# Kernel optimization log

Measured on AMD Instinct MI355X. Metric: run time of the kernel, lower is better.

## Reference

```python
import jax, jax.numpy as jnp
import numpy as np


def setup_inputs() -> dict:
    key = jax.random.key(0)
    B, L, H, D = 4, 4096, 8, 64
    sample_k = int(np.ceil(np.log(L)))  # factor=1 -> U_part = ceil(ln L_K) = 9
    k1, k2, k3, k4 = jax.random.split(key, 4)
    return {
        "queries": jax.random.normal(k1, (B, L, H, D), jnp.float32),
        "keys": jax.random.normal(k2, (B, L, H, D), jnp.float32),
        "values": jax.random.normal(k3, (B, L, H, D), jnp.float32),
        "index_sample": jax.random.randint(k4, (L, sample_k), 0, L),
    }


def _prob_attention(Q, K, V, index_sample):
    # Q, K, V: [B, H, L, D]
    B, H, L_K, D = K.shape
    L_Q = Q.shape[2]
    u = min(int(np.ceil(np.log(L_Q))), L_Q)  # n_top (static)

    # --- _prob_QK: sampled scores, sparsity measure M, top-u queries ---
    # gather sampled keys per query position: [B, H, L_Q, sample_k, D]
    K_sample = K[:, :, index_sample, :]
    QK_sample = jnp.einsum('bhld,bhlsd->bhls', Q, K_sample)  # [B,H,L_Q,S]
    M = QK_sample.max(axis=-1) - QK_sample.sum(axis=-1) / L_K  # [B,H,L_Q]
    _, M_top = jax.lax.top_k(M, u)  # [B,H,u] indices of top queries

    Q_reduce = jnp.take_along_axis(Q, M_top[..., None], axis=2)  # [B,H,u,D]
    scale = 1.0 / jnp.sqrt(jnp.asarray(D, Q.dtype))
    scores = jnp.einsum('bhud,bhkd->bhuk', Q_reduce, K) * scale  # [B,H,u,L_K]

    # --- initial context (mask_flag=False): mean of V over keys ---
    context = jnp.broadcast_to(V.mean(axis=2, keepdims=True), (B, H, L_Q, D))

    # --- update context at the top-u query positions ---
    attn = jax.nn.softmax(scores, axis=-1)  # [B,H,u,L_K]
    ctx_top = jnp.einsum('bhuk,bhkd->bhud', attn, V)  # [B,H,u,D]
    b_idx = jnp.arange(B)[:, None, None]
    h_idx = jnp.arange(H)[None, :, None]
    context = context.at[b_idx, h_idx, M_top].set(ctx_top)
    return context, attn


def reference(queries, keys, values, index_sample):
    # inputs: [B, L, H, D] -> internal [B, H, L, D]
    Q = queries.transpose(0, 2, 1, 3)
    K = keys.transpose(0, 2, 1, 3)
    V = values.transpose(0, 2, 1, 3)
    context, attn = _prob_attention(Q, K, V, index_sample)
    return context.transpose(0, 2, 1, 3), attn
```

## Files before the change

### kernel.cpp

```cpp
#include <hip/hip_runtime.h>
#include <math.h>

#define B_ 4
#define L_ 4096
#define H_ 8
#define D_ 64
#define S_ 9
#define U_ 9
#define VC_ 64
#define NC_ 32
#define CC_ 16
#define TKC_ 8

#define MBLK_ 2048
#define FILLBLK_ 8192

__device__ __forceinline__ float dot4(const float4& a, const float4& b) {
    return a.x * b.x + a.y * b.y + a.z * b.z + a.w * b.w;
}

__global__ void kernel_M_vmean(const float* __restrict__ Q, const float* __restrict__ K,
                               const int* __restrict__ idx, float* __restrict__ M,
                               const float* __restrict__ V, float* __restrict__ vpart) {
    if (blockIdx.x >= MBLK_) {
        int blk = blockIdx.x - MBLK_;
        int c = blk & (VC_ - 1), b = blk >> 6;
        int col = threadIdx.x & 127;
        int lp  = threadIdx.x >> 7;
        const int CHUNK = L_ / VC_;
        const float4* base = (const float4*)(V + (size_t)b * L_ * H_ * D_);
        float4 acc = make_float4(0.f, 0.f, 0.f, 0.f);
        for (int l = c * CHUNK + lp; l < (c + 1) * CHUNK; l += 2) {
            float4 v = base[(size_t)l * 128 + col];
            acc.x += v.x; acc.y += v.y; acc.z += v.z; acc.w += v.w;
        }
        __shared__ float4 red[256];
        red[threadIdx.x] = acc;
        __syncthreads();
        if (lp == 0) {
            float4 o = red[threadIdx.x + 128];
            acc.x += o.x; acc.y += o.y; acc.z += o.z; acc.w += o.w;
            ((float4*)vpart)[(size_t)blk * 128 + col] = acc;
        }
        return;
    }
    int n = blockIdx.x;
    int x = n & 7, m = n >> 3;
    int chunk = m & 63;
    int bh = (m >> 6) * 8 + x;
    int h = bh & (H_ - 1), b = bh >> 3;
    int t = threadIdx.x;
    int j = t & 3;
    int l = chunk * 64 + (t >> 2);

    int ki[S_];
#pragma unroll
    for (int s = 0; s < S_; ++s) ki[s] = idx[l * S_ + s];

    const float4* qb = (const float4*)(Q + (size_t)((b * L_ + l) * H_ + h) * D_);
    float4 q[4];
#pragma unroll
    for (int c = 0; c < 4; ++c) q[c] = qb[j + 4 * c];

    float dot[S_];
#pragma unroll
    for (int r = 0; r < 3; ++r) {
        const float4* kb0 = (const float4*)(K + (size_t)((b * L_ + ki[3*r+0]) * H_ + h) * D_);
        const float4* kb1 = (const float4*)(K + (size_t)((b * L_ + ki[3*r+1]) * H_ + h) * D_);
        const float4* kb2 = (const float4*)(K + (size_t)((b * L_ + ki[3*r+2]) * H_ + h) * D_);
        float4 kv0[4], kv1[4], kv2[4];
#pragma unroll
        for (int c = 0; c < 4; ++c) {
            kv0[c] = kb0[j + 4 * c];
            kv1[c] = kb1[j + 4 * c];
            kv2[c] = kb2[j + 4 * c];
        }
        float a0 = 0.f, a1 = 0.f, a2 = 0.f;
#pragma unroll
        for (int c = 0; c < 4; ++c) {
            a0 += dot4(q[c], kv0[c]);
            a1 += dot4(q[c], kv1[c]);
            a2 += dot4(q[c], kv2[c]);
        }
        dot[3*r+0] = a0; dot[3*r+1] = a1; dot[3*r+2] = a2;
    }
#pragma unroll
    for (int s = 0; s < S_; ++s) {
        dot[s] += __shfl_xor(dot[s], 1);
        dot[s] += __shfl_xor(dot[s], 2);
    }
    if (j == 0) {
        float mx = -INFINITY, sm = 0.f;
#pragma unroll
        for (int s = 0; s < S_; ++s) { mx = fmaxf(mx, dot[s]); sm += dot[s]; }
        M[((size_t)bh << 12) + l] = mx - sm * (1.0f / (float)L_);
    }
}

#define CSWAP(a, b)                                                          \
    if (v[b] > v[a] || (v[b] == v[a] && id[b] < id[a])) {                    \
        float tv = v[a]; v[a] = v[b]; v[b] = tv;                             \
        int ti = id[a]; id[a] = id[b]; id[b] = ti;                           \
    }

__global__ void kernel_topk1(const float* __restrict__ M,
                             float* __restrict__ cand_v, int* __restrict__ cand_i) {
    int bh = blockIdx.x >> 3;
    int chunk = blockIdx.x & (TKC_ - 1);
    int lane = threadIdx.x;
    const float* Ms = M + ((size_t)bh << 12);

    float v[8]; int id[8];
#pragma unroll
    for (int c = 0; c < 8; ++c) {
        int gi = chunk * 512 + lane + 64 * c;
        v[c] = Ms[gi]; id[c] = gi;
    }
    CSWAP(0,1) CSWAP(2,3) CSWAP(4,5) CSWAP(6,7)
    CSWAP(0,2) CSWAP(1,3) CSWAP(4,6) CSWAP(5,7)
    CSWAP(1,2) CSWAP(5,6)
    CSWAP(0,4) CSWAP(1,5) CSWAP(2,6) CSWAP(3,7)
    CSWAP(2,4) CSWAP(3,5)
    CSWAP(1,2) CSWAP(3,4) CSWAP(5,6)

    float* cv = cand_v + (size_t)blockIdx.x * U_;
    int*   ci = cand_i + (size_t)blockIdx.x * U_;
#pragma unroll
    for (int r = 0; r < U_; ++r) {
        float bv = v[0]; int bi = id[0];
#pragma unroll
        for (int off = 1; off < 64; off <<= 1) {
            float ov = __shfl_xor(bv, off);
            int   oi = __shfl_xor(bi, off);
            if (ov > bv || (ov == bv && oi < bi)) { bv = ov; bi = oi; }
        }
        if (lane == 0) { cv[r] = bv; ci[r] = bi; }
        if (id[0] == bi) {
#pragma unroll
            for (int c = 0; c < 7; ++c) { v[c] = v[c+1]; id[c] = id[c+1]; }
            v[7] = -INFINITY; id[7] = 0x7fffffff;
        }
    }
}

__global__ void kernel_small(const float* __restrict__ cand_v, const int* __restrict__ cand_i,
                             int* __restrict__ Mtop, const float* __restrict__ vpart,
                             float* __restrict__ vmean) {
    if (blockIdx.x >= 32) {
        int bh = blockIdx.x - 32;
        int h = bh & (H_ - 1), b = bh >> 3;
        int d = threadIdx.x;
        float s = 0.0f;
        for (int c = 0; c < VC_; ++c)
            s += vpart[(size_t)(b * VC_ + c) * (H_ * D_) + h * D_ + d];
        vmean[bh * D_ + d] = s * (1.0f / (float)L_);
        return;
    }
    int bh = blockIdx.x;
    int lane = threadIdx.x;
    const float* cv = cand_v + (size_t)bh * (TKC_ * U_);
    const int*   ci = cand_i + (size_t)bh * (TKC_ * U_);

    float v[2]; int id[2];
    v[0] = cv[lane]; id[0] = ci[lane];
    if (lane < TKC_ * U_ - 64) { v[1] = cv[64 + lane]; id[1] = ci[64 + lane]; }
    else { v[1] = -INFINITY; id[1] = 0x7fffffff; }
    CSWAP(0,1)

#pragma unroll
    for (int r = 0; r < U_; ++r) {
        float bv = v[0]; int bi = id[0];
#pragma unroll
        for (int off = 1; off < 64; off <<= 1) {
            float ov = __shfl_xor(bv, off);
            int   oi = __shfl_xor(bi, off);
            if (ov > bv || (ov == bv && oi < bi)) { bv = ov; bi = oi; }
        }
        if (lane == 0) Mtop[bh * U_ + r] = bi;
        if (id[0] == bi) { v[0] = v[1]; id[0] = id[1]; v[1] = -INFINITY; id[1] = 0x7fffffff; }
    }
}

__global__ void kernel_fill_scores(float* __restrict__ out, const float* __restrict__ vmean,
                                   const float* __restrict__ Q, const float* __restrict__ K,
                                   const int* __restrict__ Mtop, float* __restrict__ raw) {
    if (blockIdx.x < FILLBLK_) {
        int i = blockIdx.x * 256 + threadIdx.x;
        int d4 = i & 15;
        int h  = (i >> 4) & (H_ - 1);
        int b  = i >> (4 + 3 + 12);
        ((float4*)out)[i] = ((const float4*)vmean)[(b * H_ + h) * 16 + d4];
        return;
    }
    int n = blockIdx.x - FILLBLK_;
    int x = n & 7, m = n >> 3;
    int chunk = m & (NC_ - 1);
    int bh = (m >> 5) * 8 + x;
    int h = bh & (H_ - 1), b = bh >> 3;
    int k0 = chunk * (L_ / NC_);

    __shared__ float qs[U_][D_];
    int t = threadIdx.x;
    if (t < 144) {
        int u = t / 16, c = t & 15;
        int l = Mtop[bh * U_ + u];
        ((float4*)qs[u])[c] =
            ((const float4*)(Q + (size_t)((b * L_ + l) * H_ + h) * D_))[c];
    }
    __syncthreads();

    int j = t & 3, g = t >> 2;
#pragma unroll
    for (int kk = 0; kk < 2; ++kk) {
        int k = k0 + g + 64 * kk;
        const float4* kb = (const float4*)(K + (size_t)((b * L_ + k) * H_ + h) * D_);
        float4 kv[4];
#pragma unroll
        for (int c = 0; c < 4; ++c) kv[c] = kb[j + 4 * c];
#pragma unroll
        for (int u = 0; u < U_; ++u) {
            float acc = 0.0f;
#pragma unroll
            for (int c = 0; c < 4; ++c)
                acc += dot4(((const float4*)qs[u])[j + 4 * c], kv[c]);
            acc += __shfl_xor(acc, 1);
            acc += __shfl_xor(acc, 2);
            if (j == 0) raw[((size_t)bh * U_ + u) * L_ + k] = acc * 0.125f;
        }
    }
}

__global__ void kernel_softmax(float* __restrict__ attn) {
    int row = blockIdx.x;
    float4* a = (float4*)(attn + (size_t)row * L_);
    int t = threadIdx.x;

    float4 v[4];
    float mx = -INFINITY;
#pragma unroll
    for (int i = 0; i < 4; ++i) {
        v[i] = a[t + 256 * i];
        mx = fmaxf(mx, fmaxf(fmaxf(v[i].x, v[i].y), fmaxf(v[i].z, v[i].w)));
    }
    __shared__ float red[256];
    __shared__ float bmax, bsum;
    red[t] = mx;
    __syncthreads();
    for (int off = 128; off > 0; off >>= 1) {
        if (t < off) red[t] = fmaxf(red[t], red[t + off]);
        __syncthreads();
    }
    if (t == 0) bmax = red[0];
    __syncthreads();

    float mm = bmax, sum = 0.0f;
#pragma unroll
    for (int i = 0; i < 4; ++i) {
        v[i].x = expf(v[i].x - mm); v[i].y = expf(v[i].y - mm);
        v[i].z = expf(v[i].z - mm); v[i].w = expf(v[i].w - mm);
        sum += v[i].x + v[i].y + v[i].z + v[i].w;
    }
    red[t] = sum;
    __syncthreads();
    for (int off = 128; off > 0; off >>= 1) {
        if (t < off) red[t] += red[t + off];
        __syncthreads();
    }
    if (t == 0) bsum = red[0];
    __syncthreads();

    float inv = 1.0f / bsum;
#pragma unroll
    for (int i = 0; i < 4; ++i) {
        v[i].x *= inv; v[i].y *= inv; v[i].z *= inv; v[i].w *= inv;
        a[t + 256 * i] = v[i];
    }
}

__global__ void kernel_ctxf(const float* __restrict__ attn, const float* __restrict__ V,
                            float* __restrict__ cpart) {
    int n = blockIdx.x;
    int x = n & 7, m = n >> 3;
    int chunk = m & (CC_ - 1);
    int bh = (m >> 4) * 8 + x;
    int h = bh & (H_ - 1), b = bh >> 3;
    int k0 = chunk * (L_ / CC_);

    int t = threadIdx.x;
    int g = t >> 6, lane = t & 63;
    int kl = lane >> 4, d4 = lane & 15;
    const float* abase = attn + (size_t)bh * U_ * L_;

    float4 acc[U_];
#pragma unroll
    for (int u = 0; u < U_; ++u) acc[u] = make_float4(0.f, 0.f, 0.f, 0.f);

    for (int i = 0; i < 16; ++i) {
        int k = k0 + (g * 4 + kl) + 16 * i;
        float4 vv = *(const float4*)(V + (size_t)((b * L_ + k) * H_ + h) * D_ + 4 * d4);
        float av[U_];
#pragma unroll
        for (int u = 0; u < U_; ++u) av[u] = abase[(size_t)u * L_ + k];
#pragma unroll
        for (int u = 0; u < U_; ++u) {
            acc[u].x += av[u] * vv.x; acc[u].y += av[u] * vv.y;
            acc[u].z += av[u] * vv.z; acc[u].w += av[u] * vv.w;
        }
    }
#pragma unroll
    for (int u = 0; u < U_; ++u) {
        acc[u].x += __shfl_xor(acc[u].x, 16); acc[u].y += __shfl_xor(acc[u].y, 16);
        acc[u].z += __shfl_xor(acc[u].z, 16); acc[u].w += __shfl_xor(acc[u].w, 16);
        acc[u].x += __shfl_xor(acc[u].x, 32); acc[u].y += __shfl_xor(acc[u].y, 32);
        acc[u].z += __shfl_xor(acc[u].z, 32); acc[u].w += __shfl_xor(acc[u].w, 32);
    }
    __shared__ float4 red[U_][4][16];
    if (kl == 0) {
#pragma unroll
        for (int u = 0; u < U_; ++u) red[u][g][d4] = acc[u];
    }
    __syncthreads();
    if (t < U_ * 16) {
        int u = t >> 4, dd = t & 15;
        float4 s0 = red[u][0][dd], s1 = red[u][1][dd];
        float4 s2 = red[u][2][dd], s3 = red[u][3][dd];
        float4 s = make_float4(s0.x + s1.x + s2.x + s3.x, s0.y + s1.y + s2.y + s3.y,
                               s0.z + s1.z + s2.z + s3.z, s0.w + s1.w + s2.w + s3.w);
        ((float4*)cpart)[((size_t)(bh * CC_ + chunk) * U_ + u) * 16 + dd] = s;
    }
}

__global__ void kernel_ctx2(const float* __restrict__ cpart, const int* __restrict__ Mtop,
                            float* __restrict__ out) {
    int row = blockIdx.x;
    int u = row % U_, bh = row / U_;
    int h = bh & (H_ - 1), b = bh >> 3;
    int d = threadIdx.x;
    float s = 0.0f;
#pragma unroll
    for (int c = 0; c < CC_; ++c)
        s += cpart[((size_t)(bh * CC_ + c) * U_ + u) * 64 + d];
    int l = Mtop[bh * U_ + u];
    out[(size_t)((b * L_ + l) * H_ + h) * D_ + d] = s;
}

extern "C" void kernel_launch(void* const* d_in, const int* in_sizes, int n_in,
                              void* d_out, int out_size, void* d_ws, size_t ws_size,
                              hipStream_t stream) {
    const float* Q   = (const float*)d_in[0];
    const float* K   = (const float*)d_in[1];
    const float* V   = (const float*)d_in[2];
    const int*   idx = (const int*)d_in[3];

    float* ctx_out  = (float*)d_out;
    float* attn_out = (float*)d_out + (size_t)B_ * L_ * H_ * D_;

    float* M      = (float*)d_ws;
    float* vpart  = M + (size_t)B_ * H_ * L_;
    float* vmean  = vpart + (size_t)B_ * VC_ * H_ * D_;
    float* cpart  = vmean + B_ * H_ * D_;
    float* cand_v = cpart + (size_t)32 * CC_ * U_ * 64;
    int*   cand_i = (int*)(cand_v + 32 * TKC_ * U_);
    int*   Mtop   = cand_i + 32 * TKC_ * U_;

    kernel_M_vmean<<<MBLK_ + B_ * VC_, 256, 0, stream>>>(Q, K, idx, M, V, vpart);
    kernel_topk1<<<B_ * H_ * TKC_, 64, 0, stream>>>(M, cand_v, cand_i);
    kernel_small<<<64, 64, 0, stream>>>(cand_v, cand_i, Mtop, vpart, vmean);
    kernel_fill_scores<<<FILLBLK_ + 32 * NC_, 256, 0, stream>>>(ctx_out, vmean, Q, K, Mtop, attn_out);
    kernel_softmax<<<B_ * H_ * U_, 256, 0, stream>>>(attn_out);
    kernel_ctxf<<<32 * CC_, 256, 0, stream>>>(attn_out, V, cpart);
    kernel_ctx2<<<B_ * H_ * U_, 64, 0, stream>>>(cpart, Mtop, ctx_out);
}
```

Baseline: 233.0 us.

## Remap M-kernel so each wavefront handles one (b,l) row across all heads

The sampled-score kernel now assigns one wavefront per (batch, query position) and covers all 8 heads with 8 lanes each, so Q and sampled-K rows are read as contiguous 2 KB spans instead of 256-byte per-head fragments. Index loads and address math become wave-uniform via readfirstlane, and the reduction uses three shuffle stages instead of per-thread partial dots. The block count doubles to cover the new mapping. The trade is more shuffles per dot product and larger contiguous loads per lane, in exchange for better coalescing and fewer redundant index reads.

```diff
diff --git a/kernel.cpp b/kernel.cpp
--- a/kernel.cpp
+++ b/kernel.cpp
@@ -12,7 +12,7 @@
 #define CC_ 16
 #define TKC_ 8
 
-#define MBLK_ 2048
+#define MBLK_ 4096
 #define FILLBLK_ 8192
 
 __device__ __forceinline__ float dot4(const float4& a, const float4& b) {
@@ -44,56 +44,45 @@
         }
         return;
     }
-    int n = blockIdx.x;
-    int x = n & 7, m = n >> 3;
-    int chunk = m & 63;
-    int bh = (m >> 6) * 8 + x;
-    int h = bh & (H_ - 1), b = bh >> 3;
     int t = threadIdx.x;
-    int j = t & 3;
-    int l = chunk * 64 + (t >> 2);
+    int wid = t >> 6, lane = t & 63;
+    int w = (blockIdx.x << 2) + wid;
+    int b = __builtin_amdgcn_readfirstlane(w >> 12);
+    int l = __builtin_amdgcn_readfirstlane(w & (L_ - 1));
 
     int ki[S_];
 #pragma unroll
     for (int s = 0; s < S_; ++s) ki[s] = idx[l * S_ + s];
 
-    const float4* qb = (const float4*)(Q + (size_t)((b * L_ + l) * H_ + h) * D_);
-    float4 q[4];
-#pragma unroll
-    for (int c = 0; c < 4; ++c) q[c] = qb[j + 4 * c];
-
-    float dot[S_];
+    const float4* qb = (const float4*)(Q + (size_t)(b * L_ + l) * (H_ * D_));
+    float4 q0 = qb[2 * lane];
+    float4 q1 = qb[2 * lane + 1];
+
+    const float* Kb = K + (size_t)b * L_ * (H_ * D_);
+
+    float mx = -INFINITY, sm = 0.0f;
 #pragma unroll
     for (int r = 0; r < 3; ++r) {
-        const float4* kb0 = (const float4*)(K + (size_t)((b * L_ + ki[3*r+0]) * H_ + h) * D_);
-        const float4* kb1 = (const float4*)(K + (size_t)((b * L_ + ki[3*r+1]) * H_ + h) * D_);
-        const float4* kb2 = (const float4*)(K + (size_t)((b * L_ + ki[3*r+2]) * H_ + h) * D_);
-        float4 kv0[4], kv1[4], kv2[4];
-#pragma unroll
-        for (int c = 0; c < 4; ++c) {
-            kv0[c] = kb0[j + 4 * c];
-            kv1[c] = kb1[j + 4 * c];
-            kv2[c] = kb2[j + 4 * c];
-        }
-        float a0 = 0.f, a1 = 0.f, a2 = 0.f;
-#pragma unroll
-        for (int c = 0; c < 4; ++c) {
-            a0 += dot4(q[c], kv0[c]);
-            a1 += dot4(q[c], kv1[c]);
-            a2 += dot4(q[c], kv2[c]);
-        }
-        dot[3*r+0] = a0; dot[3*r+1] = a1; dot[3*r+2] = a2;
-    }
-#pragma unroll
-    for (int s = 0; s < S_; ++s) {
-        dot[s] += __shfl_xor(dot[s], 1);
-        dot[s] += __shfl_xor(dot[s], 2);
-    }
-    if (j == 0) {
-        float mx = -INFINITY, sm = 0.f;
-#pragma unroll
-        for (int s = 0; s < S_; ++s) { mx = fmaxf(mx, dot[s]); sm += dot[s]; }
-        M[((size_t)bh << 12) + l] = mx - sm * (1.0f / (float)L_);
+        float4 k0[3], k1[3];
+#pragma unroll
+        for (int i = 0; i < 3; ++i) {
+            const float4* kb = (const float4*)(Kb + (size_t)ki[3 * r + i] * (H_ * D_));
+            k0[i] = kb[2 * lane];
+            k1[i] = kb[2 * lane + 1];
+        }
+#pragma unroll
+        for (int i = 0; i < 3; ++i) {
+            float d = dot4(q0, k0[i]) + dot4(q1, k1[i]);
+            d += __shfl_xor(d, 1);
+            d += __shfl_xor(d, 2);
+            d += __shfl_xor(d, 4);
+            mx = fmaxf(mx, d);
+            sm += d;
+        }
+    }
+    if ((lane & 7) == 0) {
+        int h = lane >> 3;
+        M[((size_t)(b * H_ + h) << 12) + l] = mx - sm * (1.0f / (float)L_);
     }
 }
 
```

New measurement: 229.2 us. Within noise of the previous version (-1.6%).
